# Kernel tuning notes

Hardware: AMD Instinct MI355X
Metric: run time of the kernel (lower is better)

Reference implementation:

```python
import jax, jax.numpy as jnp
import numpy as np

IN_FEATURES = 1024
OUT_FEATURES = 1024
N_TOKENS = 32768


def setup_inputs() -> dict:
    key = jax.random.key(0)
    kx, kw, kb = jax.random.split(key, 3)
    x = jax.random.normal(kx, (N_TOKENS, IN_FEATURES), dtype=jnp.float32)
    weight = jax.random.normal(kw, (OUT_FEATURES, IN_FEATURES), dtype=jnp.float32)
    bias = jax.random.normal(kb, (OUT_FEATURES,), dtype=jnp.float32)
    return {"x": x, "weight": weight, "bias": bias}


def reference(x, weight, bias):
    # Binarize weights to {-1, 0, +1} via sign (matches torch.sign semantics),
    # then dense linear: y = x @ sign(W)^T + b
    bw = jnp.sign(weight)  # [out, in]
    return jnp.einsum('ni,oi->no', x, bw) + bias
```

## Files before the change

kernel.cpp:

```cpp
#include <hip/hip_runtime.h>
#include <stdint.h>

#define M_TOK 32768
#define N_OUT 1024
#define K_IN  1024

#define BM 128
#define BN 128
#define BK 32

typedef __bf16 bf16_t;
typedef bf16_t bf16x8 __attribute__((ext_vector_type(8)));
typedef float  floatx4 __attribute__((ext_vector_type(4)));

__device__ __forceinline__ unsigned short f2bf(float f) {
    uint32_t u = __float_as_uint(f);
    u += 0x7FFFu + ((u >> 16) & 1u);
    return (unsigned short)(u >> 16);
}

__global__ void cvt_x_kernel(const float* __restrict__ x, unsigned short* __restrict__ xb) {
    size_t i = (size_t)blockIdx.x * blockDim.x + threadIdx.x;
    const float4* xv = (const float4*)(x + i * 8);
    float4 a = xv[0];
    float4 b = xv[1];
    unsigned int p0 = (unsigned int)f2bf(a.x) | ((unsigned int)f2bf(a.y) << 16);
    unsigned int p1 = (unsigned int)f2bf(a.z) | ((unsigned int)f2bf(a.w) << 16);
    unsigned int p2 = (unsigned int)f2bf(b.x) | ((unsigned int)f2bf(b.y) << 16);
    unsigned int p3 = (unsigned int)f2bf(b.z) | ((unsigned int)f2bf(b.w) << 16);
    uint4 o; o.x = p0; o.y = p1; o.z = p2; o.w = p3;
    *(uint4*)(xb + i * 8) = o;
}

__global__ void cvt_w_kernel(const float* __restrict__ w, unsigned short* __restrict__ wb) {
    size_t i = (size_t)blockIdx.x * blockDim.x + threadIdx.x;
    const float4* wv = (const float4*)(w + i * 4);
    float4 a = wv[0];
    unsigned short s0 = (a.x > 0.f) ? 0x3F80u : ((a.x < 0.f) ? 0xBF80u : 0u);
    unsigned short s1 = (a.y > 0.f) ? 0x3F80u : ((a.y < 0.f) ? 0xBF80u : 0u);
    unsigned short s2 = (a.z > 0.f) ? 0x3F80u : ((a.z < 0.f) ? 0xBF80u : 0u);
    unsigned short s3 = (a.w > 0.f) ? 0x3F80u : ((a.w < 0.f) ? 0xBF80u : 0u);
    uint2 o;
    o.x = (unsigned int)s0 | ((unsigned int)s1 << 16);
    o.y = (unsigned int)s2 | ((unsigned int)s3 << 16);
    *(uint2*)(wb + i * 4) = o;
}

__device__ __forceinline__ void stage16(const unsigned short* gsrc, unsigned short* ldst) {
    __builtin_amdgcn_global_load_lds(
        (const __attribute__((address_space(1))) unsigned int*)gsrc,
        (__attribute__((address_space(3))) unsigned int*)ldst,
        16, 0, 0);
}

__global__ __launch_bounds__(256) void gemm_sign_kernel(
    const unsigned short* __restrict__ A,
    const unsigned short* __restrict__ B,
    const float* __restrict__ bias,
    float* __restrict__ C)
{
    __shared__ __align__(16) unsigned short sA[BM * BK];
    __shared__ __align__(16) unsigned short sB[BN * BK];

    const int t    = threadIdx.x;
    const int b    = blockIdx.x;
    const int bm   = ((b >> 6) << 3) + (b & 7);
    const int bn   = (b >> 3) & 7;

    const int wave = t >> 6;
    const int lane = t & 63;
    const int wm   = wave >> 1;
    const int wn   = wave & 1;
    const int lrow = lane & 15;
    const int quad = lane >> 4;

    const int srow = (wave << 5) + (lane >> 2);
    const int scol = (lane & 3) << 3;
    const int lds_off = (t << 3);

    unsigned short* sA0 = sA + wave * 1024 + lane * 8;
    unsigned short* sA1 = sA + wave * 1024 + 512 + lane * 8;
    unsigned short* sB0 = sB + wave * 1024 + lane * 8;
    unsigned short* sB1 = sB + wave * 1024 + 512 + lane * 8;

    const unsigned short* gA0 = A + (size_t)(bm * BM + srow)      * K_IN + scol;
    const unsigned short* gA1 = A + (size_t)(bm * BM + srow + 16) * K_IN + scol;
    const unsigned short* gB0 = B + (size_t)(bn * BN + srow)      * K_IN + scol;
    const unsigned short* gB1 = B + (size_t)(bn * BN + srow + 16) * K_IN + scol;

    floatx4 acc[4][4] = {};

    for (int kt = 0; kt < K_IN / BK; ++kt) {
        const int kbase = kt * BK;
        __syncthreads();
        stage16(gA0 + kbase, sA0);
        stage16(gA1 + kbase, sA1);
        stage16(gB0 + kbase, sB0);
        stage16(gB1 + kbase, sB1);
        __syncthreads();

        bf16x8 af[4], bfr[4];
#pragma unroll
        for (int i = 0; i < 4; ++i)
            af[i] = *(const bf16x8*)(sA + (wm * 64 + i * 16 + lrow) * BK + quad * 8);
#pragma unroll
        for (int j = 0; j < 4; ++j)
            bfr[j] = *(const bf16x8*)(sB + (wn * 64 + j * 16 + lrow) * BK + quad * 8);

#pragma unroll
        for (int i = 0; i < 4; ++i)
#pragma unroll
            for (int j = 0; j < 4; ++j)
                acc[i][j] = __builtin_amdgcn_mfma_f32_16x16x32_bf16(af[i], bfr[j], acc[i][j], 0, 0, 0);
    }

    const int crow_base = bm * BM + wm * 64;
    const int ccol_base = bn * BN + wn * 64;
#pragma unroll
    for (int j = 0; j < 4; ++j) {
        const int col = ccol_base + j * 16 + lrow;
        const float bv = bias[col];
#pragma unroll
        for (int i = 0; i < 4; ++i) {
            const int rbase = crow_base + i * 16 + quad * 4;
#pragma unroll
            for (int r = 0; r < 4; ++r) {
                C[(size_t)(rbase + r) * N_OUT + col] = acc[i][j][r] + bv;
            }
        }
    }
}

extern "C" void kernel_launch(void* const* d_in, const int* in_sizes, int n_in,
                              void* d_out, int out_size, void* d_ws, size_t ws_size,
                              hipStream_t stream) {
    const float* x    = (const float*)d_in[0];
    const float* w    = (const float*)d_in[1];
    const float* bias = (const float*)d_in[2];
    float* out        = (float*)d_out;

    unsigned short* xb = (unsigned short*)d_ws;
    unsigned short* wb = (unsigned short*)((char*)d_ws + (size_t)M_TOK * K_IN * 2);

    cvt_x_kernel<<<16384, 256, 0, stream>>>(x, xb);
    cvt_w_kernel<<<1024, 256, 0, stream>>>(w, wb);

    gemm_sign_kernel<<<(M_TOK / BM) * (N_OUT / BN), 256, 0, stream>>>(xb, wb, bias, out);
}
```

Measured before the change: 306.4 us.

## Fuse fp32-to-bf16 conversion of x into GEMM with register-prefetched tiles

Removes the separate x conversion kernel and its bf16 workspace round trip. The GEMM now loads fp32 x tiles into registers, converts them to bf16 and writes them to padded LDS (row stride 40) to reduce bank conflicts. The next tile is prefetched into registers while the MFMAs run on the current one. In exchange, fp32 x is read from global memory by every N-block (8 times) instead of bf16, which doubles A-operand traffic, and the direct global-to-LDS loads are replaced by register staging.

```diff
diff --git a/kernel.cpp b/kernel.cpp
--- a/kernel.cpp
+++ b/kernel.cpp
@@ -8,29 +8,12 @@
 #define BM 128
 #define BN 128
 #define BK 32
+#define LDT 40
 
 typedef __bf16 bf16_t;
 typedef bf16_t bf16x8 __attribute__((ext_vector_type(8)));
+typedef bf16_t bf16x4 __attribute__((ext_vector_type(4)));
 typedef float  floatx4 __attribute__((ext_vector_type(4)));
-
-__device__ __forceinline__ unsigned short f2bf(float f) {
-    uint32_t u = __float_as_uint(f);
-    u += 0x7FFFu + ((u >> 16) & 1u);
-    return (unsigned short)(u >> 16);
-}
-
-__global__ void cvt_x_kernel(const float* __restrict__ x, unsigned short* __restrict__ xb) {
-    size_t i = (size_t)blockIdx.x * blockDim.x + threadIdx.x;
-    const float4* xv = (const float4*)(x + i * 8);
-    float4 a = xv[0];
-    float4 b = xv[1];
-    unsigned int p0 = (unsigned int)f2bf(a.x) | ((unsigned int)f2bf(a.y) << 16);
-    unsigned int p1 = (unsigned int)f2bf(a.z) | ((unsigned int)f2bf(a.w) << 16);
-    unsigned int p2 = (unsigned int)f2bf(b.x) | ((unsigned int)f2bf(b.y) << 16);
-    unsigned int p3 = (unsigned int)f2bf(b.z) | ((unsigned int)f2bf(b.w) << 16);
-    uint4 o; o.x = p0; o.y = p1; o.z = p2; o.w = p3;
-    *(uint4*)(xb + i * 8) = o;
-}
 
 __global__ void cvt_w_kernel(const float* __restrict__ w, unsigned short* __restrict__ wb) {
     size_t i = (size_t)blockIdx.x * blockDim.x + threadIdx.x;
@@ -46,21 +29,14 @@
     *(uint2*)(wb + i * 4) = o;
 }
 
-__device__ __forceinline__ void stage16(const unsigned short* gsrc, unsigned short* ldst) {
-    __builtin_amdgcn_global_load_lds(
-        (const __attribute__((address_space(1))) unsigned int*)gsrc,
-        (__attribute__((address_space(3))) unsigned int*)ldst,
-        16, 0, 0);
-}
-
-__global__ __launch_bounds__(256) void gemm_sign_kernel(
-    const unsigned short* __restrict__ A,
+__global__ __launch_bounds__(256) void gemm_sign_fused(
+    const float* __restrict__ X,
     const unsigned short* __restrict__ B,
     const float* __restrict__ bias,
     float* __restrict__ C)
 {
-    __shared__ __align__(16) unsigned short sA[BM * BK];
-    __shared__ __align__(16) unsigned short sB[BN * BK];
+    __shared__ __align__(16) unsigned short sA[BM * LDT];
+    __shared__ __align__(16) unsigned short sB[BN * LDT];
 
     const int t    = threadIdx.x;
     const int b    = blockIdx.x;
@@ -74,38 +50,55 @@
     const int lrow = lane & 15;
     const int quad = lane >> 4;
 
-    const int srow = (wave << 5) + (lane >> 2);
-    const int scol = (lane & 3) << 3;
-    const int lds_off = (t << 3);
+    const int arow = t >> 3;
+    const int acol = (t & 7) * 4;
+    const float* gA = X + (size_t)(bm * BM + arow) * K_IN + acol;
+    unsigned short* sAw = sA + arow * LDT + acol;
 
-    unsigned short* sA0 = sA + wave * 1024 + lane * 8;
-    unsigned short* sA1 = sA + wave * 1024 + 512 + lane * 8;
-    unsigned short* sB0 = sB + wave * 1024 + lane * 8;
-    unsigned short* sB1 = sB + wave * 1024 + 512 + lane * 8;
+    const int brow = t >> 2;
+    const int bcol = (t & 3) * 8;
+    const unsigned short* gB = B + (size_t)(bn * BN + brow) * K_IN + bcol;
+    unsigned short* sBw = sB + brow * LDT + bcol;
 
-    const unsigned short* gA0 = A + (size_t)(bm * BM + srow)      * K_IN + scol;
-    const unsigned short* gA1 = A + (size_t)(bm * BM + srow + 16) * K_IN + scol;
-    const unsigned short* gB0 = B + (size_t)(bn * BN + srow)      * K_IN + scol;
-    const unsigned short* gB1 = B + (size_t)(bn * BN + srow + 16) * K_IN + scol;
+    floatx4 aR[4];
+    bf16x8  bR[2];
+
+    auto load_tile = [&](int kb) {
+#pragma unroll
+        for (int c = 0; c < 4; ++c)
+            aR[c] = *(const floatx4*)(gA + (size_t)c * 32 * K_IN + kb);
+#pragma unroll
+        for (int c = 0; c < 2; ++c)
+            bR[c] = *(const bf16x8*)(gB + (size_t)c * 64 * K_IN + kb);
+    };
 
     floatx4 acc[4][4] = {};
 
+    load_tile(0);
+
     for (int kt = 0; kt < K_IN / BK; ++kt) {
-        const int kbase = kt * BK;
         __syncthreads();
-        stage16(gA0 + kbase, sA0);
-        stage16(gA1 + kbase, sA1);
-        stage16(gB0 + kbase, sB0);
-        stage16(gB1 + kbase, sB1);
+
+#pragma unroll
+        for (int c = 0; c < 4; ++c) {
+            bf16x4 h = __builtin_convertvector(aR[c], bf16x4);
+            *(bf16x4*)(sAw + c * 32 * LDT) = h;
+        }
+#pragma unroll
+        for (int c = 0; c < 2; ++c)
+            *(bf16x8*)(sBw + c * 64 * LDT) = bR[c];
+
         __syncthreads();
+
+        if (kt + 1 < K_IN / BK) load_tile((kt + 1) * BK);
 
         bf16x8 af[4], bfr[4];
 #pragma unroll
         for (int i = 0; i < 4; ++i)
-            af[i] = *(const bf16x8*)(sA + (wm * 64 + i * 16 + lrow) * BK + quad * 8);
+            af[i] = *(const bf16x8*)(sA + (wm * 64 + i * 16 + lrow) * LDT + quad * 8);
 #pragma unroll
         for (int j = 0; j < 4; ++j)
-            bfr[j] = *(const bf16x8*)(sB + (wn * 64 + j * 16 + lrow) * BK + quad * 8);
+            bfr[j] = *(const bf16x8*)(sB + (wn * 64 + j * 16 + lrow) * LDT + quad * 8);
 
 #pragma unroll
         for (int i = 0; i < 4; ++i)
@@ -139,11 +132,8 @@
     const float* bias = (const float*)d_in[2];
     float* out        = (float*)d_out;
 
-    unsigned short* xb = (unsigned short*)d_ws;
-    unsigned short* wb = (unsigned short*)((char*)d_ws + (size_t)M_TOK * K_IN * 2);
+    unsigned short* wb = (unsigned short*)d_ws;
 
-    cvt_x_kernel<<<16384, 256, 0, stream>>>(x, xb);
     cvt_w_kernel<<<1024, 256, 0, stream>>>(w, wb);
-
-    gemm_sign_kernel<<<(M_TOK / BM) * (N_OUT / BN), 256, 0, stream>>>(xb, wb, bias, out);
+    gemm_sign_fused<<<(M_TOK / BM) * (N_OUT / BN), 256, 0, stream>>>(x, wb, bias, out);
 }
```

New measurement: 322.8 us. +5.4%, slower.

## Rewrite GEMM as 256x256 tile, 8-wave double-buffered pipeline with swizzled LDS

Applied to the files above, without the earlier changes.

Replaces the single-buffered 128x128x32 bf16 MFMA kernel with a 256x256x64 tile run by 8 waves. The loop is software-pipelined: global-to-LDS async loads for the next K tile are interleaved with four MFMA phases over two LDS buffers. It adds an XOR swizzle to avoid LDS bank conflicts, s_setprio around the MFMA phases, and an XCD-aware block remap. The goal is to hide global load latency and raise MFMA utilization. The cost is 128 KB of dynamic LDS, a large accumulator footprint per thread, and hand-placed waitcnt ordering that is fragile.

```diff
diff --git a/kernel.cpp b/kernel.cpp
--- a/kernel.cpp
+++ b/kernel.cpp
@@ -5,9 +5,9 @@
 #define N_OUT 1024
 #define K_IN  1024
 
-#define BM 128
-#define BN 128
-#define BK 32
+#define BM 256
+#define BN 256
+#define BK 64
 
 typedef __bf16 bf16_t;
 typedef bf16_t bf16x8 __attribute__((ext_vector_type(8)));
@@ -46,87 +46,143 @@
     *(uint2*)(wb + i * 4) = o;
 }
 
-__device__ __forceinline__ void stage16(const unsigned short* gsrc, unsigned short* ldst) {
+__device__ __forceinline__ void stage16(const unsigned short* g, unsigned short* l) {
     __builtin_amdgcn_global_load_lds(
-        (const __attribute__((address_space(1))) unsigned int*)gsrc,
-        (__attribute__((address_space(3))) unsigned int*)ldst,
-        16, 0, 0);
-}
-
-__global__ __launch_bounds__(256) void gemm_sign_kernel(
+        (const __attribute__((address_space(1))) unsigned int*)g,
+        (__attribute__((address_space(3))) unsigned int*)l, 16, 0, 0);
+}
+
+
+#define PH_OPEN() do { asm volatile("" ::: "memory"); \
+    __builtin_amdgcn_s_barrier(); \
+    __builtin_amdgcn_s_setprio(1); } while(0)
+
+#define PH_CLOSE() do { __builtin_amdgcn_s_setprio(0); \
+    asm volatile("s_waitcnt lgkmcnt(0)" ::: "memory"); \
+    __builtin_amdgcn_s_barrier(); } while(0)
+
+#define PH_CLOSE_VM() do { __builtin_amdgcn_s_setprio(0); \
+    asm volatile("s_waitcnt vmcnt(2)" ::: "memory"); \
+    asm volatile("s_waitcnt lgkmcnt(0)" ::: "memory"); \
+    __builtin_amdgcn_s_barrier(); } while(0)
+
+#define STAGE_A(p,h,kt) do { \
+    const unsigned short* _g = gAs + (size_t)((h) * 128) * K_IN + (kt) * BK; \
+    unsigned short* _l = lAs + (p) * 16384 + (h) * 8192; \
+    stage16(_g, _l); \
+    stage16(_g + (size_t)(64 * K_IN), _l + 4096); \
+} while(0)
+
+#define STAGE_B(p,h,kt) do { \
+    const unsigned short* _g = gBs + (size_t)((h) * 128) * K_IN + (kt) * BK; \
+    unsigned short* _l = lBs + (p) * 16384 + (h) * 8192; \
+    stage16(_g, _l); \
+    stage16(_g + (size_t)(64 * K_IN), _l + 4096); \
+} while(0)
+
+#define LOAD_A(p,mh) do { _Pragma("unroll") \
+    for (int mi = 0; mi < 4; ++mi) { \
+        const unsigned short* _b = rA + (p) * 16384 + ((mh) * 64 + mi * 16) * 64; \
+        af[mi][0] = *(const bf16x8*)(_b + gp0 * 8); \
+        af[mi][1] = *(const bf16x8*)(_b + gp1 * 8); \
+    } } while(0)
+
+#define LOAD_B(p,nh) do { _Pragma("unroll") \
+    for (int ni = 0; ni < 2; ++ni) { \
+        const unsigned short* _b = rB + (p) * 16384 + ((nh) * 32 + ni * 16) * 64; \
+        bf[(nh) * 2 + ni][0] = *(const bf16x8*)(_b + gp0 * 8); \
+        bf[(nh) * 2 + ni][1] = *(const bf16x8*)(_b + gp1 * 8); \
+    } } while(0)
+
+#define MFMA_Q(mh,nh) do { _Pragma("unroll") \
+    for (int mi = 0; mi < 4; ++mi) { _Pragma("unroll") \
+        for (int ni = 0; ni < 2; ++ni) { \
+            acc[(mh)*4+mi][(nh)*2+ni] = __builtin_amdgcn_mfma_f32_16x16x32_bf16( \
+                af[mi][0], bf[(nh)*2+ni][0], acc[(mh)*4+mi][(nh)*2+ni], 0, 0, 0); \
+            acc[(mh)*4+mi][(nh)*2+ni] = __builtin_amdgcn_mfma_f32_16x16x32_bf16( \
+                af[mi][1], bf[(nh)*2+ni][1], acc[(mh)*4+mi][(nh)*2+ni], 0, 0, 0); \
+        } } } while(0)
+
+__global__ __launch_bounds__(512, 2) void gemm8p(
     const unsigned short* __restrict__ A,
     const unsigned short* __restrict__ B,
     const float* __restrict__ bias,
     float* __restrict__ C)
 {
-    __shared__ __align__(16) unsigned short sA[BM * BK];
-    __shared__ __align__(16) unsigned short sB[BN * BK];
-
-    const int t    = threadIdx.x;
-    const int b    = blockIdx.x;
-    const int bm   = ((b >> 6) << 3) + (b & 7);
-    const int bn   = (b >> 3) & 7;
-
-    const int wave = t >> 6;
+    extern __shared__ unsigned short lds[];
+    unsigned short* sA = lds;
+    unsigned short* sB = lds + 32768;
+
+    const int t = threadIdx.x;
+    const int b = blockIdx.x;
+    const int wg = ((b & 7) << 6) + (b >> 3);
+    const int bm = wg >> 2;
+    const int bn = wg & 3;
+
+    const int w    = t >> 6;
     const int lane = t & 63;
-    const int wm   = wave >> 1;
-    const int wn   = wave & 1;
+    const int wm   = w >> 2;
+    const int wn   = w & 3;
     const int lrow = lane & 15;
     const int quad = lane >> 4;
 
-    const int srow = (wave << 5) + (lane >> 2);
-    const int scol = (lane & 3) << 3;
-    const int lds_off = (t << 3);
-
-    unsigned short* sA0 = sA + wave * 1024 + lane * 8;
-    unsigned short* sA1 = sA + wave * 1024 + 512 + lane * 8;
-    unsigned short* sB0 = sB + wave * 1024 + lane * 8;
-    unsigned short* sB1 = sB + wave * 1024 + 512 + lane * 8;
-
-    const unsigned short* gA0 = A + (size_t)(bm * BM + srow)      * K_IN + scol;
-    const unsigned short* gA1 = A + (size_t)(bm * BM + srow + 16) * K_IN + scol;
-    const unsigned short* gB0 = B + (size_t)(bn * BN + srow)      * K_IN + scol;
-    const unsigned short* gB1 = B + (size_t)(bn * BN + srow + 16) * K_IN + scol;
-
-    floatx4 acc[4][4] = {};
-
-    for (int kt = 0; kt < K_IN / BK; ++kt) {
-        const int kbase = kt * BK;
-        __syncthreads();
-        stage16(gA0 + kbase, sA0);
-        stage16(gA1 + kbase, sA1);
-        stage16(gB0 + kbase, sB0);
-        stage16(gB1 + kbase, sB1);
-        __syncthreads();
-
-        bf16x8 af[4], bfr[4];
+    const int srow = (w << 3) + (lane >> 3);
+    const int glog = (lane & 7) ^ (lane >> 3);
+    const unsigned short* gAs = A + (size_t)(bm * BM + srow) * K_IN + glog * 8;
+    const unsigned short* gBs = B + (size_t)(bn * BN + srow) * K_IN + glog * 8;
+    unsigned short* lAs = sA + t * 8;
+    unsigned short* lBs = sB + t * 8;
+
+    const unsigned short* rA = sA + wm * 8192 + lrow * 64;
+    const unsigned short* rB = sB + (wn >> 1) * 8192 + ((wn & 1) * 64 + lrow) * 64;
+    const int gp0 = quad ^ (lrow & 7);
+    const int gp1 = (4 + quad) ^ (lrow & 7);
+
+    bf16x8  af[4][2];
+    bf16x8  bf[4][2];
+    floatx4 acc[8][4] = {};
+
+    STAGE_A(0, 0, 0); STAGE_A(0, 1, 0); STAGE_B(0, 0, 0); STAGE_B(0, 1, 0);
+    STAGE_A(1, 0, 1);
+    asm volatile("s_waitcnt vmcnt(2)" ::: "memory");
+    __builtin_amdgcn_s_barrier();
+
+#pragma unroll 1
+    for (int i = 0; i < 8; ++i) {
+        const int t1 = 2 * i + 1;
+        const int e  = (2 * i + 2) & 15;
+        const int o  = (2 * i + 3) & 15;
+        LOAD_A(0, 0); LOAD_B(0, 0); STAGE_A(1, 1, t1);
+        PH_OPEN(); MFMA_Q(0, 0); PH_CLOSE();
+        LOAD_B(0, 1); STAGE_B(1, 0, t1);
+        PH_OPEN(); MFMA_Q(0, 1); PH_CLOSE();
+        LOAD_A(0, 1); STAGE_B(1, 1, t1);
+        PH_OPEN(); MFMA_Q(1, 0); PH_CLOSE();
+        STAGE_A(0, 0, e);
+        PH_OPEN(); MFMA_Q(1, 1); PH_CLOSE_VM();
+        LOAD_A(1, 0); LOAD_B(1, 0); STAGE_A(0, 1, e);
+        PH_OPEN(); MFMA_Q(0, 0); PH_CLOSE();
+        LOAD_B(1, 1); STAGE_B(0, 0, e);
+        PH_OPEN(); MFMA_Q(0, 1); PH_CLOSE();
+        LOAD_A(1, 1); STAGE_B(0, 1, e);
+        PH_OPEN(); MFMA_Q(1, 0); PH_CLOSE();
+        STAGE_A(1, 0, o);
+        PH_OPEN(); MFMA_Q(1, 1); PH_CLOSE_VM();
+    }
+    asm volatile("s_waitcnt vmcnt(0)" ::: "memory");
+
+    const int crow0 = bm * BM + wm * 128 + quad * 4;
+    const int ccol0 = bn * BN + wn * 64;
 #pragma unroll
-        for (int i = 0; i < 4; ++i)
-            af[i] = *(const bf16x8*)(sA + (wm * 64 + i * 16 + lrow) * BK + quad * 8);
-#pragma unroll
-        for (int j = 0; j < 4; ++j)
-            bfr[j] = *(const bf16x8*)(sB + (wn * 64 + j * 16 + lrow) * BK + quad * 8);
-
-#pragma unroll
-        for (int i = 0; i < 4; ++i)
-#pragma unroll
-            for (int j = 0; j < 4; ++j)
-                acc[i][j] = __builtin_amdgcn_mfma_f32_16x16x32_bf16(af[i], bfr[j], acc[i][j], 0, 0, 0);
-    }
-
-    const int crow_base = bm * BM + wm * 64;
-    const int ccol_base = bn * BN + wn * 64;
-#pragma unroll
-    for (int j = 0; j < 4; ++j) {
-        const int col = ccol_base + j * 16 + lrow;
+    for (int ni = 0; ni < 4; ++ni) {
+        const int col = ccol0 + ni * 16 + lrow;
         const float bv = bias[col];
 #pragma unroll
-        for (int i = 0; i < 4; ++i) {
-            const int rbase = crow_base + i * 16 + quad * 4;
+        for (int mi = 0; mi < 8; ++mi) {
+            const int row = crow0 + mi * 16;
 #pragma unroll
-            for (int r = 0; r < 4; ++r) {
-                C[(size_t)(rbase + r) * N_OUT + col] = acc[i][j][r] + bv;
-            }
+            for (int r = 0; r < 4; ++r)
+                C[(size_t)(row + r) * N_OUT + col] = acc[mi][ni][r] + bv;
         }
     }
 }
@@ -142,8 +198,14 @@
     unsigned short* xb = (unsigned short*)d_ws;
     unsigned short* wb = (unsigned short*)((char*)d_ws + (size_t)M_TOK * K_IN * 2);
 
+    static bool attr_set = false;
+    if (!attr_set) {
+        hipFuncSetAttribute((const void*)gemm8p,
+                            hipFuncAttributeMaxDynamicSharedMemorySize, 131072);
+        attr_set = true;
+    }
+
     cvt_x_kernel<<<16384, 256, 0, stream>>>(x, xb);
     cvt_w_kernel<<<1024, 256, 0, stream>>>(w, wb);
-
-    gemm_sign_kernel<<<(M_TOK / BM) * (N_OUT / BN), 256, 0, stream>>>(xb, wb, bias, out);
-}
+    gemm8p<<<(M_TOK / BM) * (N_OUT / BN), 512, 131072, stream>>>(xb, wb, bias, out);
+}
```

New measurement: 302.7 us. No clear change (-1.2%).
